# Performance work log

Measured on AMD Instinct MI355X. Metric: run time of the kernel, lower is better.

The kernel has to match this reference:

```python
import jax, jax.numpy as jnp
import numpy as np

E, H, S, NH, B = 32768, 256, 32, 8, 64
HD = H // NH


def setup_inputs() -> dict:
    key = jax.random.key(0)
    ks = jax.random.split(key, 13)
    sc = 1.0 / np.sqrt(H)
    return {
        "edge_features": jax.random.normal(ks[0], (E, H), jnp.float32),
        "edge_coords": jax.random.normal(ks[1], (E, 3), jnp.float32),
        "batch": jnp.sort(jax.random.randint(ks[2], (E,), 0, B, dtype=jnp.int32)),
        "seed_vectors": jax.random.normal(ks[3], (S, H), jnp.float32),
        "Wq": jax.random.normal(ks[4], (H, H), jnp.float32) * sc,
        "Wk": jax.random.normal(ks[5], (H, H), jnp.float32) * sc,
        "Wv": jax.random.normal(ks[6], (H, H), jnp.float32) * sc,
        "Wo": jax.random.normal(ks[7], (H, H), jnp.float32) * sc,
        "bo": jnp.zeros((H,), jnp.float32),
        "W1": jax.random.normal(ks[8], (H, S * H), jnp.float32) / np.sqrt(S * H),
        "b1": jnp.zeros((H,), jnp.float32),
        "W2": jax.random.normal(ks[9], (H, H), jnp.float32) * sc,
        "b2": jnp.zeros((H,), jnp.float32),
    }


def reference(edge_features, edge_coords, batch, seed_vectors,
              Wq, Wk, Wv, Wo, bo, W1, b1, W2, b2):
    # Per-graph PMA cross-attention: shared seed queries attend over each
    # graph's ragged set of edges (segment softmax), then out_proj + MLP.
    # edge_coords is unused by the original forward.
    q = (seed_vectors @ Wq.T).reshape(S, NH, HD)          # [S, nh, hd]
    k = (edge_features @ Wk.T).reshape(E, NH, HD)         # [E, nh, hd]
    v = (edge_features @ Wv.T).reshape(E, NH, HD)         # [E, nh, hd]

    scores = jnp.einsum('shd,ehd->ehs', q, k) / (HD ** 0.5)   # [E, nh, S]
    # segment (per-graph) stable softmax over the edge axis
    smax = jax.ops.segment_max(scores, batch, num_segments=B,
                               indices_are_sorted=True)        # [B, nh, S]
    ex = jnp.exp(scores - smax[batch])
    denom = jax.ops.segment_sum(ex, batch, num_segments=B,
                                indices_are_sorted=True)       # [B, nh, S]
    w = ex / denom[batch]                                      # [E, nh, S]

    # attended[b, nh, S, hd] = sum_{e in graph b} w[e,nh,S] * v[e,nh,hd]
    attended = jax.ops.segment_sum(w[:, :, :, None] * v[:, :, None, :],
                                   batch, num_segments=B,
                                   indices_are_sorted=True)    # [B, nh, S, hd]
    attended = attended.transpose(0, 2, 1, 3).reshape(B, S, H)  # [B, S, H]

    graph_repr = attended @ Wo.T + bo                           # [B, S, H]
    flat = graph_repr.reshape(B, S * H)
    h1 = jax.nn.silu(flat @ W1.T + b1)                          # [B, H]
    return h1 @ W2.T + b2                                       # [B, H]
```

## Files before the change

### kernel.cpp

```cpp
#include <hip/hip_runtime.h>
#include <hip/hip_bf16.h>

#define E_N 32768
#define H_N 256
#define S_N 32
#define NH_N 8
#define B_N 64

typedef _Float16 f16x8 __attribute__((ext_vector_type(8)));
typedef _Float16 f16x4 __attribute__((ext_vector_type(4)));
typedef float    f32x4 __attribute__((ext_vector_type(4)));

#define OFF_MTH    0
#define OFF_MM     65536
#define OFF_DI     81920
#define OFF_MP     98304
#define OFF_SP     622592
#define OFF_ATT4   98304
#define OFF_ATT    2195456
#define OFF_GR     2719744
#define OFF_PART   3244032
#define OFF_H1     4292608
#define OFF_SCORES 4308992
#define OFF_VH     12697600

__device__ inline int lower_bound64(const int* __restrict__ batch, int b) {
    int lo = 0, hi = E_N;
    while (lo < hi) { int mid = (lo + hi) >> 1; if (batch[mid] < b) lo = mid + 1; else hi = mid; }
    return lo;
}

__global__ __launch_bounds__(256) void prep(const float* __restrict__ seed,
                                            const float* __restrict__ Wq,
                                            const float* __restrict__ Wk,
                                            const float* __restrict__ Wv,
                                            _Float16* __restrict__ Mth) {
    const int t = threadIdx.x, bid = blockIdx.x;
    if (bid < 8) {
        const int nh = bid;
        __shared__ float q_l[32][32];
        const int d = t & 31, s0 = t >> 5;
        float a0 = 0, a1 = 0, a2 = 0, a3 = 0;
        const float* wq = &Wq[(nh * 32 + d) * 256];
        for (int j = 0; j < 256; ++j) {
            float w = wq[j];
            a0 += w * seed[(s0) * 256 + j];
            a1 += w * seed[(s0 + 8) * 256 + j];
            a2 += w * seed[(s0 + 16) * 256 + j];
            a3 += w * seed[(s0 + 24) * 256 + j];
        }
        q_l[s0][d] = a0; q_l[s0 + 8][d] = a1; q_l[s0 + 16][d] = a2; q_l[s0 + 24][d] = a3;
        __syncthreads();
        float acc[32];
#pragma unroll
        for (int s = 0; s < 32; ++s) acc[s] = 0.f;
        for (int dd = 0; dd < 32; ++dd) {
            float w = Wk[(nh * 32 + dd) * 256 + t];
#pragma unroll
            for (int s = 0; s < 32; ++s) acc[s] += w * q_l[s][dd];
        }
        const float scale = 0.17677669529663687f;
        for (int s = 0; s < 32; ++s)
            Mth[(nh * 32 + s) * 256 + t] = (_Float16)(acc[s] * scale);
    } else {
        const int j0 = (bid - 8) * 32;
        for (int jj = 0; jj < 32; ++jj)
            Mth[(256 + j0 + jj) * 256 + t] = (_Float16)Wv[(j0 + jj) * 256 + t];
    }
}

__global__ __launch_bounds__(256) void gemm16(const float* __restrict__ X,
                                              const _Float16* __restrict__ Mth,
                                              float* __restrict__ scores,
                                              _Float16* __restrict__ vh) {
    __shared__ _Float16 As[128][72];
    __shared__ _Float16 Bs[128][72];
    const int tid = threadIdx.x;
    const int n0 = blockIdx.x * 128;
    const int m0 = blockIdx.y * 128;
    const int w = tid >> 6, l = tid & 63;
    const int lr = l & 15, kg = l >> 4;
    const int wr = (w & 1) * 64, wc = (w >> 1) * 64;
    f32x4 acc[4][4] = {};

    for (int ks = 0; ks < 4; ++ks) {
        const int k0 = ks * 64;
#pragma unroll
        for (int i = 0; i < 8; ++i) {
            int idx = tid + i * 256;
            int row = idx >> 4, c4 = (idx & 15) * 4;
            float4 xv = *(const float4*)&X[(m0 + row) * 256 + k0 + c4];
            f16x4 h;
            h[0] = (_Float16)xv.x; h[1] = (_Float16)xv.y;
            h[2] = (_Float16)xv.z; h[3] = (_Float16)xv.w;
            *(f16x4*)&As[row][c4] = h;
        }
#pragma unroll
        for (int i = 0; i < 4; ++i) {
            int idx = tid + i * 256;
            int row = idx >> 3, c8 = (idx & 7) * 8;
            *(uint4*)&Bs[row][c8] = *(const uint4*)&Mth[(n0 + row) * 256 + k0 + c8];
        }
        __syncthreads();
#pragma unroll
        for (int kk = 0; kk < 2; ++kk) {
            f16x8 af[4], bf[4];
#pragma unroll
            for (int mr = 0; mr < 4; ++mr)
                af[mr] = *(const f16x8*)&As[wr + mr * 16 + lr][kk * 32 + kg * 8];
#pragma unroll
            for (int nc = 0; nc < 4; ++nc)
                bf[nc] = *(const f16x8*)&Bs[wc + nc * 16 + lr][kk * 32 + kg * 8];
#pragma unroll
            for (int mr = 0; mr < 4; ++mr)
#pragma unroll
                for (int nc = 0; nc < 4; ++nc)
                    acc[mr][nc] = __builtin_amdgcn_mfma_f32_16x16x32_f16(
                        af[mr], bf[nc], acc[mr][nc], 0, 0, 0);
        }
        __syncthreads();
    }
    const int r0 = m0 + wr + kg * 4;
    if (n0 < 256) {
#pragma unroll
        for (int mr = 0; mr < 4; ++mr)
#pragma unroll
            for (int nc = 0; nc < 4; ++nc) {
                int col = n0 + wc + nc * 16 + lr;
#pragma unroll
                for (int j = 0; j < 4; ++j)
                    scores[(r0 + mr * 16 + j) * 256 + col] = acc[mr][nc][j];
            }
    } else {
#pragma unroll
        for (int mr = 0; mr < 4; ++mr)
#pragma unroll
            for (int nc = 0; nc < 4; ++nc) {
                int col = n0 - 256 + wc + nc * 16 + lr;
#pragma unroll
                for (int j = 0; j < 4; ++j)
                    vh[(r0 + mr * 16 + j) * 256 + col] = (_Float16)acc[mr][nc][j];
            }
    }
}

__global__ __launch_bounds__(256) void stats_partial(const float* __restrict__ scores,
                                                     const int* __restrict__ batch,
                                                     float* __restrict__ mp,
                                                     float* __restrict__ sp) {
    const int b = blockIdx.x, c = blockIdx.y, t = threadIdx.x;
    const int e0 = lower_bound64(batch, b);
    const int e1 = lower_bound64(batch, b + 1);
    const int len = e1 - e0;
    const int cs = e0 + (len * c) / 32;
    const int ce = e0 + (len * (c + 1)) / 32;
    float m0 = -3.4e38f, m1 = -3.4e38f, m2 = -3.4e38f, m3 = -3.4e38f;
    int e = cs;
    for (; e + 4 <= ce; e += 4) {
        m0 = fmaxf(m0, scores[(e + 0) * 256 + t]);
        m1 = fmaxf(m1, scores[(e + 1) * 256 + t]);
        m2 = fmaxf(m2, scores[(e + 2) * 256 + t]);
        m3 = fmaxf(m3, scores[(e + 3) * 256 + t]);
    }
    for (; e < ce; ++e) m0 = fmaxf(m0, scores[e * 256 + t]);
    float m = fmaxf(fmaxf(m0, m1), fmaxf(m2, m3));
    float s0 = 0.f, s1 = 0.f, s2 = 0.f, s3 = 0.f;
    e = cs;
    for (; e + 4 <= ce; e += 4) {
        s0 += __expf(scores[(e + 0) * 256 + t] - m);
        s1 += __expf(scores[(e + 1) * 256 + t] - m);
        s2 += __expf(scores[(e + 2) * 256 + t] - m);
        s3 += __expf(scores[(e + 3) * 256 + t] - m);
    }
    for (; e < ce; ++e) s0 += __expf(scores[e * 256 + t] - m);
    mp[(b * 32 + c) * 256 + t] = m;
    sp[(b * 32 + c) * 256 + t] = (s0 + s1) + (s2 + s3);
}

__global__ __launch_bounds__(256) void stats_merge(const float* __restrict__ mp,
                                                   const float* __restrict__ sp,
                                                   float* __restrict__ mm,
                                                   float* __restrict__ di) {
    const int b = blockIdx.x, t = threadIdx.x;
    float m = -3.4e38f;
#pragma unroll
    for (int c = 0; c < 32; ++c) m = fmaxf(m, mp[(b * 32 + c) * 256 + t]);
    float d = 0.f;
#pragma unroll
    for (int c = 0; c < 32; ++c) {
        float sc = sp[(b * 32 + c) * 256 + t];
        if (sc > 0.f) d += sc * __expf(mp[(b * 32 + c) * 256 + t] - m);
    }
    mm[b * 256 + t] = m;
    di[b * 256 + t] = (d > 0.f) ? 1.f / d : 0.f;
}

__global__ __launch_bounds__(256) void attend(const float* __restrict__ scores,
                                              const _Float16* __restrict__ vh,
                                              const int* __restrict__ batch,
                                              const float* __restrict__ mm,
                                              const float* __restrict__ di,
                                              float* __restrict__ att4) {
    const int b = blockIdx.x, nh = blockIdx.y, c = blockIdx.z, t = threadIdx.x;
    const int e0 = lower_bound64(batch, b);
    const int e1 = lower_bound64(batch, b + 1);
    const int len = e1 - e0;
    const int cs = e0 + (len * c) / 4;
    const int ce = e0 + (len * (c + 1)) / 4;
    __shared__ float wl[32][33];
    __shared__ float vl[32][33];
    __shared__ float mc[32], dc[32];
    if (t < 32) {
        mc[t] = mm[b * 256 + nh * 32 + t];
        dc[t] = di[b * 256 + nh * 32 + t];
    }
    __syncthreads();
    const int s = t & 31, g = t >> 5;
    const int le = t >> 3, q = t & 7;
    float acc0 = 0.f, acc1 = 0.f, acc2 = 0.f, acc3 = 0.f;
    for (int te = cs; te < ce; te += 32) {
        const int e = te + le;
        const bool ok = (e < ce);
        float4 x = make_float4(0.f, 0.f, 0.f, 0.f);
        f16x4 vv = {};
        if (ok) {
            x = *(const float4*)&scores[e * 256 + nh * 32 + q * 4];
            vv = *(const f16x4*)&vh[e * 256 + nh * 32 + q * 4];
        }
        wl[le][q * 4 + 0] = ok ? __expf(x.x - mc[q * 4 + 0]) : 0.f;
        wl[le][q * 4 + 1] = ok ? __expf(x.y - mc[q * 4 + 1]) : 0.f;
        wl[le][q * 4 + 2] = ok ? __expf(x.z - mc[q * 4 + 2]) : 0.f;
        wl[le][q * 4 + 3] = ok ? __expf(x.w - mc[q * 4 + 3]) : 0.f;
        vl[le][q * 4 + 0] = ok ? (float)vv[0] : 0.f;
        vl[le][q * 4 + 1] = ok ? (float)vv[1] : 0.f;
        vl[le][q * 4 + 2] = ok ? (float)vv[2] : 0.f;
        vl[le][q * 4 + 3] = ok ? (float)vv[3] : 0.f;
        __syncthreads();
#pragma unroll
        for (int e2 = 0; e2 < 32; ++e2) {
            float wv = wl[e2][s];
            acc0 += wv * vl[e2][g * 4 + 0];
            acc1 += wv * vl[e2][g * 4 + 1];
            acc2 += wv * vl[e2][g * 4 + 2];
            acc3 += wv * vl[e2][g * 4 + 3];
        }
        __syncthreads();
    }
    const float dv = dc[s];
    float* op = &att4[((size_t)c * 2048 + b * 32 + s) * 256 + nh * 32 + g * 4];
    op[0] = acc0 * dv; op[1] = acc1 * dv; op[2] = acc2 * dv; op[3] = acc3 * dv;
}

__global__ __launch_bounds__(256) void attend_reduce(const float* __restrict__ att4,
                                                     float* __restrict__ att) {
    const int i = (blockIdx.x * 256 + threadIdx.x) * 4;
    float4 a = *(const float4*)&att4[i];
    float4 b = *(const float4*)&att4[524288 + i];
    float4 c = *(const float4*)&att4[2 * 524288 + i];
    float4 d = *(const float4*)&att4[3 * 524288 + i];
    *(float4*)&att[i] = make_float4(a.x + b.x + c.x + d.x, a.y + b.y + c.y + d.y,
                                    a.z + b.z + c.z + d.z, a.w + b.w + c.w + d.w);
}

__global__ __launch_bounds__(256) void gemm_abT(const float* __restrict__ A,
                                                const float* __restrict__ W,
                                                const float* __restrict__ bias,
                                                float* __restrict__ out0) {
    __shared__ float As[16][64];
    __shared__ float Bs[16][64];
    const int tid = threadIdx.x;
    const int m0 = blockIdx.y * 64, n0 = blockIdx.x * 64;
    const int tx = tid & 15, ty = tid >> 4;
    const int lrow = tid >> 2;
    const int lkq = (tid & 3) * 4;
    float acc[4][4];
#pragma unroll
    for (int i = 0; i < 4; ++i)
#pragma unroll
        for (int j = 0; j < 4; ++j) acc[i][j] = 0.f;

    for (int k0 = 0; k0 < 256; k0 += 16) {
        float4 av = *(const float4*)&A[(m0 + lrow) * 256 + k0 + lkq];
        float4 wv = *(const float4*)&W[(n0 + lrow) * 256 + k0 + lkq];
        As[lkq + 0][lrow] = av.x; As[lkq + 1][lrow] = av.y;
        As[lkq + 2][lrow] = av.z; As[lkq + 3][lrow] = av.w;
        Bs[lkq + 0][lrow] = wv.x; Bs[lkq + 1][lrow] = wv.y;
        Bs[lkq + 2][lrow] = wv.z; Bs[lkq + 3][lrow] = wv.w;
        __syncthreads();
#pragma unroll
        for (int k = 0; k < 16; ++k) {
            float4 a4 = *(const float4*)&As[k][ty * 4];
            float4 b4 = *(const float4*)&Bs[k][tx * 4];
            acc[0][0] += a4.x * b4.x; acc[0][1] += a4.x * b4.y;
            acc[0][2] += a4.x * b4.z; acc[0][3] += a4.x * b4.w;
            acc[1][0] += a4.y * b4.x; acc[1][1] += a4.y * b4.y;
            acc[1][2] += a4.y * b4.z; acc[1][3] += a4.y * b4.w;
            acc[2][0] += a4.z * b4.x; acc[2][1] += a4.z * b4.y;
            acc[2][2] += a4.z * b4.z; acc[2][3] += a4.z * b4.w;
            acc[3][0] += a4.w * b4.x; acc[3][1] += a4.w * b4.y;
            acc[3][2] += a4.w * b4.z; acc[3][3] += a4.w * b4.w;
        }
        __syncthreads();
    }
    const int c = n0 + tx * 4;
    float4 bb = bias ? *(const float4*)&bias[c]
                     : make_float4(0.f, 0.f, 0.f, 0.f);
#pragma unroll
    for (int mi = 0; mi < 4; ++mi) {
        int r = m0 + ty * 4 + mi;
        float4 o = make_float4(acc[mi][0] + bb.x, acc[mi][1] + bb.y,
                               acc[mi][2] + bb.z, acc[mi][3] + bb.w);
        *(float4*)&out0[r * 256 + c] = o;
    }
}

__global__ __launch_bounds__(256) void gemm_w1_splitk(const float* __restrict__ flat,
                                                      const float* __restrict__ W1,
                                                      float* __restrict__ partials) {
    __shared__ float As[16][64];
    __shared__ float Bs[16][64];
    const int tid = threadIdx.x;
    const int n0 = blockIdx.x * 64;
    const int kbase = blockIdx.y * 128;
    const int tx = tid & 15, ty = tid >> 4;
    const int lrow = tid >> 2, lkq = (tid & 3) * 4;
    float acc[4][4];
#pragma unroll
    for (int i = 0; i < 4; ++i)
#pragma unroll
        for (int j = 0; j < 4; ++j) acc[i][j] = 0.f;

    for (int k0 = 0; k0 < 128; k0 += 16) {
        float4 av = *(const float4*)&flat[lrow * 8192 + kbase + k0 + lkq];
        float4 wv = *(const float4*)&W1[(n0 + lrow) * 8192 + kbase + k0 + lkq];
        As[lkq + 0][lrow] = av.x; As[lkq + 1][lrow] = av.y;
        As[lkq + 2][lrow] = av.z; As[lkq + 3][lrow] = av.w;
        Bs[lkq + 0][lrow] = wv.x; Bs[lkq + 1][lrow] = wv.y;
        Bs[lkq + 2][lrow] = wv.z; Bs[lkq + 3][lrow] = wv.w;
        __syncthreads();
#pragma unroll
        for (int k = 0; k < 16; ++k) {
            float4 a4 = *(const float4*)&As[k][ty * 4];
            float4 b4 = *(const float4*)&Bs[k][tx * 4];
            acc[0][0] += a4.x * b4.x; acc[0][1] += a4.x * b4.y;
            acc[0][2] += a4.x * b4.z; acc[0][3] += a4.x * b4.w;
            acc[1][0] += a4.y * b4.x; acc[1][1] += a4.y * b4.y;
            acc[1][2] += a4.y * b4.z; acc[1][3] += a4.y * b4.w;
            acc[2][0] += a4.z * b4.x; acc[2][1] += a4.z * b4.y;
            acc[2][2] += a4.z * b4.z; acc[2][3] += a4.z * b4.w;
            acc[3][0] += a4.w * b4.x; acc[3][1] += a4.w * b4.y;
            acc[3][2] += a4.w * b4.z; acc[3][3] += a4.w * b4.w;
        }
        __syncthreads();
    }
#pragma unroll
    for (int mi = 0; mi < 4; ++mi) {
        int bb = ty * 4 + mi;
        *(float4*)&partials[blockIdx.y * 16384 + bb * 256 + n0 + tx * 4] =
            make_float4(acc[mi][0], acc[mi][1], acc[mi][2], acc[mi][3]);
    }
}

__global__ void silu_reduce(const float* __restrict__ partials,
                            const float* __restrict__ b1,
                            float* __restrict__ h1) {
    int t = blockIdx.x * 256 + threadIdx.x;
    float s0 = b1[t & 255], s1 = 0.f, s2 = 0.f, s3 = 0.f;
#pragma unroll
    for (int ks = 0; ks < 64; ks += 4) {
        s0 += partials[(ks + 0) * 16384 + t];
        s1 += partials[(ks + 1) * 16384 + t];
        s2 += partials[(ks + 2) * 16384 + t];
        s3 += partials[(ks + 3) * 16384 + t];
    }
    float sum = (s0 + s1) + (s2 + s3);
    h1[t] = sum / (1.f + __expf(-sum));
}

extern "C" void kernel_launch(void* const* d_in, const int* in_sizes, int n_in,
                              void* d_out, int out_size, void* d_ws, size_t ws_size,
                              hipStream_t stream) {
    const float* X     = (const float*)d_in[0];
    const int*   batch = (const int*)d_in[2];
    const float* seed  = (const float*)d_in[3];
    const float* Wq    = (const float*)d_in[4];
    const float* Wk    = (const float*)d_in[5];
    const float* Wv    = (const float*)d_in[6];
    const float* Wo    = (const float*)d_in[7];
    const float* bo    = (const float*)d_in[8];
    const float* W1    = (const float*)d_in[9];
    const float* b1    = (const float*)d_in[10];
    const float* W2    = (const float*)d_in[11];
    const float* b2    = (const float*)d_in[12];
    float* out = (float*)d_out;
    float* ws = (float*)d_ws;

    _Float16* Mth   = (_Float16*)(ws + OFF_MTH);
    float* mm       = ws + OFF_MM;
    float* di       = ws + OFF_DI;
    float* mp       = ws + OFF_MP;
    float* sp       = ws + OFF_SP;
    float* att4     = ws + OFF_ATT4;
    float* att      = ws + OFF_ATT;
    float* gr       = ws + OFF_GR;
    float* part     = ws + OFF_PART;
    float* h1       = ws + OFF_H1;
    float* scores   = ws + OFF_SCORES;
    _Float16* vh    = (_Float16*)(ws + OFF_VH);

    hipLaunchKernelGGL(prep, dim3(16), dim3(256), 0, stream, seed, Wq, Wk, Wv, Mth);
    hipLaunchKernelGGL(gemm16, dim3(4, 256), dim3(256), 0, stream, X, Mth, scores, vh);
    hipLaunchKernelGGL(stats_partial, dim3(64, 32), dim3(256), 0, stream, scores, batch, mp, sp);
    hipLaunchKernelGGL(stats_merge, dim3(64), dim3(256), 0, stream, mp, sp, mm, di);
    hipLaunchKernelGGL(attend, dim3(64, 8, 4), dim3(256), 0, stream, scores, vh, batch, mm, di, att4);
    hipLaunchKernelGGL(attend_reduce, dim3(512), dim3(256), 0, stream, att4, att);
    hipLaunchKernelGGL(gemm_abT, dim3(4, 32), dim3(256), 0, stream, att, Wo, bo, gr);
    hipLaunchKernelGGL(gemm_w1_splitk, dim3(4, 64), dim3(256), 0, stream, gr, W1, part);
    hipLaunchKernelGGL(silu_reduce, dim3(64), dim3(256), 0, stream, part, b1, h1);
    hipLaunchKernelGGL(gemm_abT, dim3(4, 1), dim3(256), 0, stream, h1, W2, b2, out);
}
```

Measured before the change: 247.5 us.

## Pre-convert X to fp16, fuse attend reduce into Wo GEMM, tune small kernels

Adds a separate kernel that converts edge features to fp16 once, so the main GEMM loads half-width tiles directly. The four-way partial reduction of attended values moves into the Wo projection's A-tile load, which drops a kernel and its intermediate buffer. The prep kernel now stages seed vectors in shared memory with vectorized Wq loads, and the final W2 GEMM is replaced by a simple dot-product kernel with 64 blocks. The fp16 conversion costs an extra full read plus a half-size write of X and adds one launch, and the Wo GEMM now reads four times more A data.

```diff
diff --git a/kernel.cpp b/kernel.cpp
--- a/kernel.cpp
+++ b/kernel.cpp
@@ -17,17 +17,28 @@
 #define OFF_MP     98304
 #define OFF_SP     622592
 #define OFF_ATT4   98304
-#define OFF_ATT    2195456
-#define OFF_GR     2719744
-#define OFF_PART   3244032
-#define OFF_H1     4292608
-#define OFF_SCORES 4308992
-#define OFF_VH     12697600
+#define OFF_GR     2195456
+#define OFF_PART   2719744
+#define OFF_H1     3768320
+#define OFF_SCORES 3784704
+#define OFF_VH     12173312
+#define OFF_XH     14270464
 
 __device__ inline int lower_bound64(const int* __restrict__ batch, int b) {
     int lo = 0, hi = E_N;
     while (lo < hi) { int mid = (lo + hi) >> 1; if (batch[mid] < b) lo = mid + 1; else hi = mid; }
     return lo;
+}
+
+__global__ __launch_bounds__(256) void xcvt(const float* __restrict__ X,
+                                            _Float16* __restrict__ Xh) {
+    const int i = (blockIdx.x * 256 + threadIdx.x) * 8;
+    float4 a = *(const float4*)&X[i];
+    float4 b = *(const float4*)&X[i + 4];
+    f16x8 h;
+    h[0] = (_Float16)a.x; h[1] = (_Float16)a.y; h[2] = (_Float16)a.z; h[3] = (_Float16)a.w;
+    h[4] = (_Float16)b.x; h[5] = (_Float16)b.y; h[6] = (_Float16)b.z; h[7] = (_Float16)b.w;
+    *(f16x8*)&Xh[i] = h;
 }
 
 __global__ __launch_bounds__(256) void prep(const float* __restrict__ seed,
@@ -36,18 +47,26 @@
                                             const float* __restrict__ Wv,
                                             _Float16* __restrict__ Mth) {
     const int t = threadIdx.x, bid = blockIdx.x;
+    __shared__ float sld[32][256];
+    __shared__ float q_l[32][32];
     if (bid < 8) {
         const int nh = bid;
-        __shared__ float q_l[32][32];
+        for (int i = t; i < 2048; i += 256) {
+            int r = i >> 6, c4 = (i & 63) * 4;
+            *(float4*)&sld[r][c4] = *(const float4*)&seed[r * 256 + c4];
+        }
+        __syncthreads();
         const int d = t & 31, s0 = t >> 5;
+        const float4* wq4 = (const float4*)&Wq[(nh * 32 + d) * 256];
         float a0 = 0, a1 = 0, a2 = 0, a3 = 0;
-        const float* wq = &Wq[(nh * 32 + d) * 256];
-        for (int j = 0; j < 256; ++j) {
-            float w = wq[j];
-            a0 += w * seed[(s0) * 256 + j];
-            a1 += w * seed[(s0 + 8) * 256 + j];
-            a2 += w * seed[(s0 + 16) * 256 + j];
-            a3 += w * seed[(s0 + 24) * 256 + j];
+#pragma unroll 8
+        for (int j4 = 0; j4 < 64; ++j4) {
+            float4 w = wq4[j4];
+            const int j = j4 * 4;
+            a0 += w.x * sld[s0][j] + w.y * sld[s0][j + 1] + w.z * sld[s0][j + 2] + w.w * sld[s0][j + 3];
+            a1 += w.x * sld[s0 + 8][j] + w.y * sld[s0 + 8][j + 1] + w.z * sld[s0 + 8][j + 2] + w.w * sld[s0 + 8][j + 3];
+            a2 += w.x * sld[s0 + 16][j] + w.y * sld[s0 + 16][j + 1] + w.z * sld[s0 + 16][j + 2] + w.w * sld[s0 + 16][j + 3];
+            a3 += w.x * sld[s0 + 24][j] + w.y * sld[s0 + 24][j + 1] + w.z * sld[s0 + 24][j + 2] + w.w * sld[s0 + 24][j + 3];
         }
         q_l[s0][d] = a0; q_l[s0 + 8][d] = a1; q_l[s0 + 16][d] = a2; q_l[s0 + 24][d] = a3;
         __syncthreads();
@@ -69,7 +88,7 @@
     }
 }
 
-__global__ __launch_bounds__(256) void gemm16(const float* __restrict__ X,
+__global__ __launch_bounds__(256) void gemm16(const _Float16* __restrict__ Xh,
                                               const _Float16* __restrict__ Mth,
                                               float* __restrict__ scores,
                                               _Float16* __restrict__ vh) {
@@ -86,14 +105,10 @@
     for (int ks = 0; ks < 4; ++ks) {
         const int k0 = ks * 64;
 #pragma unroll
-        for (int i = 0; i < 8; ++i) {
+        for (int i = 0; i < 4; ++i) {
             int idx = tid + i * 256;
-            int row = idx >> 4, c4 = (idx & 15) * 4;
-            float4 xv = *(const float4*)&X[(m0 + row) * 256 + k0 + c4];
-            f16x4 h;
-            h[0] = (_Float16)xv.x; h[1] = (_Float16)xv.y;
-            h[2] = (_Float16)xv.z; h[3] = (_Float16)xv.w;
-            *(f16x4*)&As[row][c4] = h;
+            int row = idx >> 3, c8 = (idx & 7) * 8;
+            *(uint4*)&As[row][c8] = *(const uint4*)&Xh[(m0 + row) * 256 + k0 + c8];
         }
 #pragma unroll
         for (int i = 0; i < 4; ++i) {
@@ -247,25 +262,14 @@
         __syncthreads();
     }
     const float dv = dc[s];
-    float* op = &att4[((size_t)c * 2048 + b * 32 + s) * 256 + nh * 32 + g * 4];
+    float* op = &att4[((size_t)c * 524288) + (b * 32 + s) * 256 + nh * 32 + g * 4];
     op[0] = acc0 * dv; op[1] = acc1 * dv; op[2] = acc2 * dv; op[3] = acc3 * dv;
 }
 
-__global__ __launch_bounds__(256) void attend_reduce(const float* __restrict__ att4,
-                                                     float* __restrict__ att) {
-    const int i = (blockIdx.x * 256 + threadIdx.x) * 4;
-    float4 a = *(const float4*)&att4[i];
-    float4 b = *(const float4*)&att4[524288 + i];
-    float4 c = *(const float4*)&att4[2 * 524288 + i];
-    float4 d = *(const float4*)&att4[3 * 524288 + i];
-    *(float4*)&att[i] = make_float4(a.x + b.x + c.x + d.x, a.y + b.y + c.y + d.y,
-                                    a.z + b.z + c.z + d.z, a.w + b.w + c.w + d.w);
-}
-
-__global__ __launch_bounds__(256) void gemm_abT(const float* __restrict__ A,
-                                                const float* __restrict__ W,
-                                                const float* __restrict__ bias,
-                                                float* __restrict__ out0) {
+__global__ __launch_bounds__(256) void gemm_wo(const float* __restrict__ att4,
+                                               const float* __restrict__ W,
+                                               const float* __restrict__ bias,
+                                               float* __restrict__ out0) {
     __shared__ float As[16][64];
     __shared__ float Bs[16][64];
     const int tid = threadIdx.x;
@@ -280,7 +284,13 @@
         for (int j = 0; j < 4; ++j) acc[i][j] = 0.f;
 
     for (int k0 = 0; k0 < 256; k0 += 16) {
-        float4 av = *(const float4*)&A[(m0 + lrow) * 256 + k0 + lkq];
+        const int ai = (m0 + lrow) * 256 + k0 + lkq;
+        float4 a0 = *(const float4*)&att4[ai];
+        float4 a1 = *(const float4*)&att4[524288 + ai];
+        float4 a2 = *(const float4*)&att4[2 * 524288 + ai];
+        float4 a3 = *(const float4*)&att4[3 * 524288 + ai];
+        float4 av = make_float4(a0.x + a1.x + a2.x + a3.x, a0.y + a1.y + a2.y + a3.y,
+                                a0.z + a1.z + a2.z + a3.z, a0.w + a1.w + a2.w + a3.w);
         float4 wv = *(const float4*)&W[(n0 + lrow) * 256 + k0 + lkq];
         As[lkq + 0][lrow] = av.x; As[lkq + 1][lrow] = av.y;
         As[lkq + 2][lrow] = av.z; As[lkq + 3][lrow] = av.w;
@@ -303,8 +313,7 @@
         __syncthreads();
     }
     const int c = n0 + tx * 4;
-    float4 bb = bias ? *(const float4*)&bias[c]
-                     : make_float4(0.f, 0.f, 0.f, 0.f);
+    float4 bb = *(const float4*)&bias[c];
 #pragma unroll
     for (int mi = 0; mi < 4; ++mi) {
         int r = m0 + ty * 4 + mi;
@@ -375,6 +384,29 @@
     }
     float sum = (s0 + s1) + (s2 + s3);
     h1[t] = sum / (1.f + __expf(-sum));
+}
+
+__global__ __launch_bounds__(256) void gemm_w2(const float* __restrict__ h1,
+                                               const float* __restrict__ W2,
+                                               const float* __restrict__ b2,
+                                               float* __restrict__ out) {
+    const int t = threadIdx.x;
+    const int b = t & 63, cc = blockIdx.x * 4 + (t >> 6);
+    const float4* hv = (const float4*)&h1[b * 256];
+    const float4* wv = (const float4*)&W2[cc * 256];
+    float a0 = 0, a1 = 0, a2 = 0, a3 = 0;
+#pragma unroll 8
+    for (int k = 0; k < 64; k += 4) {
+        float4 h0 = hv[k + 0], w0 = wv[k + 0];
+        a0 += h0.x * w0.x + h0.y * w0.y + h0.z * w0.z + h0.w * w0.w;
+        float4 h1_ = hv[k + 1], w1 = wv[k + 1];
+        a1 += h1_.x * w1.x + h1_.y * w1.y + h1_.z * w1.z + h1_.w * w1.w;
+        float4 h2 = hv[k + 2], w2 = wv[k + 2];
+        a2 += h2.x * w2.x + h2.y * w2.y + h2.z * w2.z + h2.w * w2.w;
+        float4 h3 = hv[k + 3], w3 = wv[k + 3];
+        a3 += h3.x * w3.x + h3.y * w3.y + h3.z * w3.z + h3.w * w3.w;
+    }
+    out[b * 256 + cc] = (a0 + a1) + (a2 + a3) + b2[cc];
 }
 
 extern "C" void kernel_launch(void* const* d_in, const int* in_sizes, int n_in,
@@ -401,21 +433,21 @@
     float* mp       = ws + OFF_MP;
     float* sp       = ws + OFF_SP;
     float* att4     = ws + OFF_ATT4;
-    float* att      = ws + OFF_ATT;
     float* gr       = ws + OFF_GR;
     float* part     = ws + OFF_PART;
     float* h1       = ws + OFF_H1;
     float* scores   = ws + OFF_SCORES;
     _Float16* vh    = (_Float16*)(ws + OFF_VH);
+    _Float16* Xh    = (_Float16*)(ws + OFF_XH);
 
     hipLaunchKernelGGL(prep, dim3(16), dim3(256), 0, stream, seed, Wq, Wk, Wv, Mth);
-    hipLaunchKernelGGL(gemm16, dim3(4, 256), dim3(256), 0, stream, X, Mth, scores, vh);
+    hipLaunchKernelGGL(xcvt, dim3(4096), dim3(256), 0, stream, X, Xh);
+    hipLaunchKernelGGL(gemm16, dim3(4, 256), dim3(256), 0, stream, Xh, Mth, scores, vh);
     hipLaunchKernelGGL(stats_partial, dim3(64, 32), dim3(256), 0, stream, scores, batch, mp, sp);
     hipLaunchKernelGGL(stats_merge, dim3(64), dim3(256), 0, stream, mp, sp, mm, di);
     hipLaunchKernelGGL(attend, dim3(64, 8, 4), dim3(256), 0, stream, scores, vh, batch, mm, di, att4);
-    hipLaunchKernelGGL(attend_reduce, dim3(512), dim3(256), 0, stream, att4, att);
-    hipLaunchKernelGGL(gemm_abT, dim3(4, 32), dim3(256), 0, stream, att, Wo, bo, gr);
+    hipLaunchKernelGGL(gemm_wo, dim3(4, 32), dim3(256), 0, stream, att4, Wo, bo, gr);
     hipLaunchKernelGGL(gemm_w1_splitk, dim3(4, 64), dim3(256), 0, stream, gr, W1, part);
     hipLaunchKernelGGL(silu_reduce, dim3(64), dim3(256), 0, stream, part, b1, h1);
-    hipLaunchKernelGGL(gemm_abT, dim3(4, 1), dim3(256), 0, stream, h1, W2, b2, out);
-}
+    hipLaunchKernelGGL(gemm_w2, dim3(64), dim3(256), 0, stream, h1, W2, b2, out);
+}
```

Result: faster. 234.9 us (-5.1%).
